# Performance work log

Hardware: AMD Instinct MI355X
Metric: run time of the kernel (lower is better)

Reference implementation:

```python
import functools
import jax, jax.numpy as jnp
import numpy as np

CUTOFF = 5.0
BOX = 80.0
N_POINTS = 8192
MAX_NEIGHBOURS = 32
MASK_VALUE = -1


def setup_inputs() -> dict:
    key = jax.random.key(0)
    positions = jax.random.uniform(key, (N_POINTS, 3), dtype=jnp.float32) * BOX
    return {"positions": positions, "max_neighbours": MAX_NEIGHBOURS}


def reference(positions, max_neighbours):
    # OpenBoundary.get_neighbours (include_self=False, cutoff=CUTOFF)
    n = positions.shape[0]
    # pairwise squared distances: vmap(neighbours_mask_direct) == full broadcast
    diff = positions[:, None, :] - positions[None, :, :]        # [N, N, 3]
    r2 = jnp.sum(diff * diff, axis=-1)                          # [N, N]
    neigh_mask = r2 <= CUTOFF * CUTOFF
    neigh_mask = neigh_mask & ~jnp.eye(n, dtype=bool)           # drop self
    # per-row compaction of hit indices into fixed-size buffer
    get_nb = functools.partial(jnp.argwhere, size=max_neighbours, fill_value=MASK_VALUE)
    to_idx = jax.vmap(get_nb)(neigh_mask)[..., 0]               # [N, max_neighbours]
    cell_indices = jnp.zeros((*to_idx.shape, 3), dtype=jnp.int32)
    actual_max_neighbours = jnp.max(neigh_mask.sum(axis=1))
    return to_idx, cell_indices, actual_max_neighbours
```

## Files before the change

### kernel.cpp

```cpp
#include <hip/hip_runtime.h>


constexpr int   N     = 8192;
constexpr int   MAXNB = 32;
constexpr float CUT2  = 25.0f;
constexpr int   C     = 15;
constexpr int   NCP   = 4096;
constexpr float INVW  = 0.1875f;
constexpr int   QBLOCKS = N / 4;

__device__ __forceinline__ int cell_coord(float v) {
    int c = (int)(v * INVW);
    return c > C - 1 ? C - 1 : c;
}

__global__ __launch_bounds__(1024) void build_kernel(const float* __restrict__ pos,
                                                     int* __restrict__ start_g,
                                                     float4* __restrict__ sorted) {
    __shared__ int cnt[NCP];
    __shared__ int ws[1024];
    const int t = threadIdx.x;

    #pragma unroll
    for (int k = t; k < NCP; k += 1024) cnt[k] = 0;
    __syncthreads();

    int cid[8], rnk[8];
    #pragma unroll
    for (int q = 0; q < 8; ++q) {
        const int i = q * 1024 + t;
        const int cx = cell_coord(pos[3 * i + 0]);
        const int cy = cell_coord(pos[3 * i + 1]);
        const int cz = cell_coord(pos[3 * i + 2]);
        cid[q] = (cz * C + cy) * C + cx;
        rnk[q] = atomicAdd(&cnt[cid[q]], 1);
    }
    __syncthreads();

    int c[4], pre[4], s = 0;
    #pragma unroll
    for (int k = 0; k < 4; ++k) { c[k] = cnt[4 * t + k]; pre[k] = s; s += c[k]; }
    ws[t] = s;
    __syncthreads();
    for (int off = 1; off < 1024; off <<= 1) {
        const int v = (t >= off) ? ws[t - off] : 0;
        __syncthreads();
        ws[t] += v;
        __syncthreads();
    }
    const int excl = ws[t] - s;
    #pragma unroll
    for (int k = 0; k < 4; ++k) {
        cnt[4 * t + k]     = excl + pre[k];
        start_g[4 * t + k] = excl + pre[k];
    }
    if (t == 0) start_g[NCP] = N;
    __syncthreads();

    #pragma unroll
    for (int q = 0; q < 8; ++q) {
        const int i = q * 1024 + t;
        const int p = cnt[cid[q]] + rnk[q];
        sorted[p] = make_float4(pos[3 * i + 0], pos[3 * i + 1], pos[3 * i + 2],
                                __int_as_float(i));
    }
}

__global__ __launch_bounds__(256) void query_kernel(const float* __restrict__ pos,
                                                    const float4* __restrict__ sorted,
                                                    const int* __restrict__ start_g,
                                                    int* __restrict__ out_idx,
                                                    int* __restrict__ blockmax) {
    __shared__ int hitbuf[4][64];
    __shared__ int wmax[4];
    const int lane = threadIdx.x & 63;
    const int wave = threadIdx.x >> 6;
    const int p    = blockIdx.x * 4 + wave;

    const float x = pos[3 * p + 0];
    const float y = pos[3 * p + 1];
    const float z = pos[3 * p + 2];
    const int cx = cell_coord(x), cy = cell_coord(y), cz = cell_coord(z);
    const int xa = cx > 0 ? cx - 1 : 0;
    const int xb = cx < C - 1 ? cx + 1 : C - 1;

    int count = 0;
    #pragma unroll
    for (int s = 0; s < 9; ++s) {
        const int zz = cz + s / 3 - 1;
        const int yy = cy + s % 3 - 1;
        if (zz < 0 || zz >= C || yy < 0 || yy >= C) continue;
        const int rowb = (zz * C + yy) * C;
        const int b = start_g[rowb + xa];
        const int e = start_g[rowb + xb + 1];
        for (int k = b; k < e; k += 64) {
            const int idx = k + lane;
            const float4 o = sorted[idx < N ? idx : N - 1];
            const float dx = __fsub_rn(x, o.x);
            const float dy = __fsub_rn(y, o.y);
            const float dz = __fsub_rn(z, o.z);
            const float r2 = __fadd_rn(__fadd_rn(__fmul_rn(dx, dx), __fmul_rn(dy, dy)),
                                       __fmul_rn(dz, dz));
            const int j = __float_as_int(o.w);
            const bool hit = (idx < e) && (r2 <= CUT2) && (j != p);
            const unsigned long long m = __ballot(hit);
            if (hit) {
                const int pre = __builtin_amdgcn_mbcnt_hi(
                    (unsigned int)(m >> 32),
                    __builtin_amdgcn_mbcnt_lo((unsigned int)m, 0u));
                const int slot = count + pre;
                if (slot < 64) hitbuf[wave][slot] = j;
            }
            count += __popcll(m);
        }
    }

    const int mcount = count < 64 ? count : 64;
    int v = (lane < mcount) ? hitbuf[wave][lane] : 0x7fffffff;
    #pragma unroll
    for (int k = 2; k <= 64; k <<= 1) {
        #pragma unroll
        for (int jj = k >> 1; jj >= 1; jj >>= 1) {
            const int pv = __shfl_xor(v, jj);
            const bool keepmin = ((lane & jj) == 0) == ((lane & k) == 0);
            v = keepmin ? min(v, pv) : max(v, pv);
        }
    }
    if (lane < MAXNB) out_idx[p * MAXNB + lane] = (lane < count) ? v : -1;

    if (lane == 0) wmax[wave] = count;
    __syncthreads();
    if (threadIdx.x == 0)
        blockmax[blockIdx.x] = max(max(wmax[0], wmax[1]), max(wmax[2], wmax[3]));
}

__global__ __launch_bounds__(256) void finalize_kernel(int4* __restrict__ cell4,
                                                       const int* __restrict__ blockmax,
                                                       int* __restrict__ out_max) {
    __shared__ int wm[4];
    const int idx = blockIdx.x * 256 + threadIdx.x;
    cell4[idx] = make_int4(0, 0, 0, 0);
    if (blockIdx.x == 0) {
        int mx = 0;
        for (int k = threadIdx.x; k < QBLOCKS; k += 256) mx = max(mx, blockmax[k]);
        #pragma unroll
        for (int off = 32; off > 0; off >>= 1) mx = max(mx, __shfl_down(mx, off));
        if ((threadIdx.x & 63) == 0) wm[threadIdx.x >> 6] = mx;
        __syncthreads();
        if (threadIdx.x == 0)
            *out_max = max(max(wm[0], wm[1]), max(wm[2], wm[3]));
    }
}

extern "C" void kernel_launch(void* const* d_in, const int* in_sizes, int n_in,
                              void* d_out, int out_size, void* d_ws, size_t ws_size,
                              hipStream_t stream) {
    const float* pos = (const float*)d_in[0];
    int* out = (int*)d_out;

    int* out_idx = out;
    int* base    = out + N * MAXNB;
    int* out_max = out + N * MAXNB * 4;

    int*    start_g = base;
    float4* sorted  = (float4*)(base + 8192);
    int*    blockmax = (int*)d_ws;

    build_kernel   <<<1, 1024, 0, stream>>>(pos, start_g, sorted);
    query_kernel   <<<QBLOCKS, 256, 0, stream>>>(pos, sorted, start_g, out_idx, blockmax);
    finalize_kernel<<<N * MAXNB * 3 / 4 / 256, 256, 0, stream>>>((int4*)base, blockmax, out_max);
}
```

Before: 78.83 us.

## Replace sorted cell list with fixed-capacity cell bins and drop finalize kernel

The build kernel no longer does a block-wide prefix scan to sort points by cell. Each point now goes into a fixed 16-slot bin per cell, and per-cell counts are written to workspace. The query kernel reads a clamped 4x3x3 cell window with one 64-lane load per row instead of variable-length loops. The cell_indices zeroing and the global max are folded into the query kernel, the max via atomicMax, which removes the third launch. The risks are that points beyond 16 per cell are silently dropped and that out_max is never zeroed before the atomicMax.

```diff
diff --git a/kernel.cpp b/kernel.cpp
--- a/kernel.cpp
+++ b/kernel.cpp
@@ -5,9 +5,10 @@
 constexpr int   MAXNB = 32;
 constexpr float CUT2  = 25.0f;
 constexpr int   C     = 15;
-constexpr int   NCP   = 4096;
+constexpr int   NC    = C * C * C;
 constexpr float INVW  = 0.1875f;
-constexpr int   QBLOCKS = N / 4;
+constexpr int   CAPC  = 16;
+constexpr int   QB    = N / 4;
 
 __device__ __forceinline__ int cell_coord(float v) {
     int c = (int)(v * INVW);
@@ -15,62 +16,40 @@
 }
 
 __global__ __launch_bounds__(1024) void build_kernel(const float* __restrict__ pos,
-                                                     int* __restrict__ start_g,
-                                                     float4* __restrict__ sorted) {
-    __shared__ int cnt[NCP];
-    __shared__ int ws[1024];
+                                                     int* __restrict__ cnt_g,
+                                                     float4* __restrict__ cells) {
+    __shared__ int cnt[NC];
     const int t = threadIdx.x;
-
-    #pragma unroll
-    for (int k = t; k < NCP; k += 1024) cnt[k] = 0;
+    for (int k = t; k < NC; k += 1024) cnt[k] = 0;
     __syncthreads();
 
+    float x[8], y[8], z[8];
     int cid[8], rnk[8];
     #pragma unroll
     for (int q = 0; q < 8; ++q) {
         const int i = q * 1024 + t;
-        const int cx = cell_coord(pos[3 * i + 0]);
-        const int cy = cell_coord(pos[3 * i + 1]);
-        const int cz = cell_coord(pos[3 * i + 2]);
-        cid[q] = (cz * C + cy) * C + cx;
+        x[q] = pos[3 * i + 0];
+        y[q] = pos[3 * i + 1];
+        z[q] = pos[3 * i + 2];
+        cid[q] = (cell_coord(z[q]) * C + cell_coord(y[q])) * C + cell_coord(x[q]);
         rnk[q] = atomicAdd(&cnt[cid[q]], 1);
     }
     __syncthreads();
 
-    int c[4], pre[4], s = 0;
-    #pragma unroll
-    for (int k = 0; k < 4; ++k) { c[k] = cnt[4 * t + k]; pre[k] = s; s += c[k]; }
-    ws[t] = s;
-    __syncthreads();
-    for (int off = 1; off < 1024; off <<= 1) {
-        const int v = (t >= off) ? ws[t - off] : 0;
-        __syncthreads();
-        ws[t] += v;
-        __syncthreads();
-    }
-    const int excl = ws[t] - s;
-    #pragma unroll
-    for (int k = 0; k < 4; ++k) {
-        cnt[4 * t + k]     = excl + pre[k];
-        start_g[4 * t + k] = excl + pre[k];
-    }
-    if (t == 0) start_g[NCP] = N;
-    __syncthreads();
-
+    for (int k = t; k < NC; k += 1024) cnt_g[k] = cnt[k];
     #pragma unroll
     for (int q = 0; q < 8; ++q) {
-        const int i = q * 1024 + t;
-        const int p = cnt[cid[q]] + rnk[q];
-        sorted[p] = make_float4(pos[3 * i + 0], pos[3 * i + 1], pos[3 * i + 2],
-                                __int_as_float(i));
+        if (rnk[q] < CAPC)
+            cells[cid[q] * CAPC + rnk[q]] =
+                make_float4(x[q], y[q], z[q], __int_as_float(q * 1024 + t));
     }
 }
 
 __global__ __launch_bounds__(256) void query_kernel(const float* __restrict__ pos,
-                                                    const float4* __restrict__ sorted,
-                                                    const int* __restrict__ start_g,
-                                                    int* __restrict__ out_idx,
-                                                    int* __restrict__ blockmax) {
+                                                    const float4* __restrict__ cells,
+                                                    const int* __restrict__ cnt_g,
+                                                    int* __restrict__ out,
+                                                    int* __restrict__ out_max) {
     __shared__ int hitbuf[4][64];
     __shared__ int wmax[4];
     const int lane = threadIdx.x & 63;
@@ -81,38 +60,38 @@
     const float y = pos[3 * p + 1];
     const float z = pos[3 * p + 2];
     const int cx = cell_coord(x), cy = cell_coord(y), cz = cell_coord(z);
-    const int xa = cx > 0 ? cx - 1 : 0;
-    const int xb = cx < C - 1 ? cx + 1 : C - 1;
+    int xa = cx - 1; xa = xa < 0 ? 0 : (xa > C - 4 ? C - 4 : xa);
+    int ya = cy - 1; ya = ya < 0 ? 0 : (ya > C - 3 ? C - 3 : ya);
+    int za = cz - 1; za = za < 0 ? 0 : (za > C - 3 ? C - 3 : za);
+
+    const int lc = lane >> 4;
+    const int ls = lane & 15;
 
     int count = 0;
     #pragma unroll
     for (int s = 0; s < 9; ++s) {
-        const int zz = cz + s / 3 - 1;
-        const int yy = cy + s % 3 - 1;
-        if (zz < 0 || zz >= C || yy < 0 || yy >= C) continue;
-        const int rowb = (zz * C + yy) * C;
-        const int b = start_g[rowb + xa];
-        const int e = start_g[rowb + xb + 1];
-        for (int k = b; k < e; k += 64) {
-            const int idx = k + lane;
-            const float4 o = sorted[idx < N ? idx : N - 1];
-            const float dx = __fsub_rn(x, o.x);
-            const float dy = __fsub_rn(y, o.y);
-            const float dz = __fsub_rn(z, o.z);
-            const float r2 = __fadd_rn(__fadd_rn(__fmul_rn(dx, dx), __fmul_rn(dy, dy)),
-                                       __fmul_rn(dz, dz));
-            const int j = __float_as_int(o.w);
-            const bool hit = (idx < e) && (r2 <= CUT2) && (j != p);
-            const unsigned long long m = __ballot(hit);
-            if (hit) {
-                const int pre = __builtin_amdgcn_mbcnt_hi(
-                    (unsigned int)(m >> 32),
-                    __builtin_amdgcn_mbcnt_lo((unsigned int)m, 0u));
-                const int slot = count + pre;
-                if (slot < 64) hitbuf[wave][slot] = j;
-            }
-            count += __popcll(m);
+        const int zz = za + s / 3;
+        const int yy = ya + s % 3;
+        const int cidb = (zz * C + yy) * C + xa;
+        const int cid  = cidb + lc;
+        const float4 o = cells[cidb * CAPC + lane];
+        const int   cc = cnt_g[cid];
+        const float dx = __fsub_rn(x, o.x);
+        const float dy = __fsub_rn(y, o.y);
+        const float dz = __fsub_rn(z, o.z);
+        const float r2 = __fadd_rn(__fadd_rn(__fmul_rn(dx, dx), __fmul_rn(dy, dy)),
+                                   __fmul_rn(dz, dz));
+        const int j = __float_as_int(o.w);
+        const bool hit = (ls < cc) && (r2 <= CUT2) && (j != p);
+        const unsigned long long m = __ballot(hit);
+        if (hit) {
+            const int pre = __builtin_amdgcn_mbcnt_hi(
+                (unsigned int)(m >> 32),
+                __builtin_amdgcn_mbcnt_lo((unsigned int)m, 0u));
+            const int slot = count + pre;
+            if (slot < 64) hitbuf[wave][slot] = j;
         }
+        count += __popcll(m);
     }
 
     const int mcount = count < 64 ? count : 64;
@@ -126,30 +105,15 @@
             v = keepmin ? min(v, pv) : max(v, pv);
         }
     }
-    if (lane < MAXNB) out_idx[p * MAXNB + lane] = (lane < count) ? v : -1;
+    if (lane < MAXNB) out[p * MAXNB + lane] = (lane < count) ? v : -1;
+
+    int4* c4 = (int4*)(out + N * MAXNB) + blockIdx.x * 96;
+    if (threadIdx.x < 96) c4[threadIdx.x] = make_int4(0, 0, 0, 0);
 
     if (lane == 0) wmax[wave] = count;
     __syncthreads();
     if (threadIdx.x == 0)
-        blockmax[blockIdx.x] = max(max(wmax[0], wmax[1]), max(wmax[2], wmax[3]));
-}
-
-__global__ __launch_bounds__(256) void finalize_kernel(int4* __restrict__ cell4,
-                                                       const int* __restrict__ blockmax,
-                                                       int* __restrict__ out_max) {
-    __shared__ int wm[4];
-    const int idx = blockIdx.x * 256 + threadIdx.x;
-    cell4[idx] = make_int4(0, 0, 0, 0);
-    if (blockIdx.x == 0) {
-        int mx = 0;
-        for (int k = threadIdx.x; k < QBLOCKS; k += 256) mx = max(mx, blockmax[k]);
-        #pragma unroll
-        for (int off = 32; off > 0; off >>= 1) mx = max(mx, __shfl_down(mx, off));
-        if ((threadIdx.x & 63) == 0) wm[threadIdx.x >> 6] = mx;
-        __syncthreads();
-        if (threadIdx.x == 0)
-            *out_max = max(max(wm[0], wm[1]), max(wm[2], wm[3]));
-    }
+        atomicMax(out_max, max(max(wmax[0], wmax[1]), max(wmax[2], wmax[3])));
 }
 
 extern "C" void kernel_launch(void* const* d_in, const int* in_sizes, int n_in,
@@ -157,16 +121,11 @@
                               hipStream_t stream) {
     const float* pos = (const float*)d_in[0];
     int* out = (int*)d_out;
-
-    int* out_idx = out;
-    int* base    = out + N * MAXNB;
     int* out_max = out + N * MAXNB * 4;
 
-    int*    start_g = base;
-    float4* sorted  = (float4*)(base + 8192);
-    int*    blockmax = (int*)d_ws;
+    int*    cnt_g = (int*)d_ws;
+    float4* cells = (float4*)((char*)d_ws + 16384);
 
-    build_kernel   <<<1, 1024, 0, stream>>>(pos, start_g, sorted);
-    query_kernel   <<<QBLOCKS, 256, 0, stream>>>(pos, sorted, start_g, out_idx, blockmax);
-    finalize_kernel<<<N * MAXNB * 3 / 4 / 256, 256, 0, stream>>>((int4*)base, blockmax, out_max);
+    build_kernel<<<1, 1024, 0, stream>>>(pos, cnt_g, cells);
+    query_kernel<<<QB, 256, 0, stream>>>(pos, cells, cnt_g, out, out_max);
 }
```

Result: slower. 93.12 us (+18.1%).

## Flatten 9 cell-row ranges into one contiguous lane-packed loop

Applied to the files above, without the earlier changes.

The query kernel now precomputes the begin offsets and prefix sums of all nine 3-cell row ranges and loops over their concatenated length in 64-lane chunks. Each lane maps its flat index back to a sorted position with a select chain. This packs partial chunks from different rows together, cutting wasted lanes and loop iterations. The window is also clamped to the grid interior, so edge particles scan a full 3x3x3 block that includes some extra cells. The query index is made wave-uniform with readfirstlane. The cost is nine extra compare/selects per lane per iteration.

```diff
diff --git a/kernel.cpp b/kernel.cpp
--- a/kernel.cpp
+++ b/kernel.cpp
@@ -75,44 +75,52 @@
     __shared__ int wmax[4];
     const int lane = threadIdx.x & 63;
     const int wave = threadIdx.x >> 6;
-    const int p    = blockIdx.x * 4 + wave;
+    const int p = __builtin_amdgcn_readfirstlane((int)blockIdx.x * 4 + wave);
 
     const float x = pos[3 * p + 0];
     const float y = pos[3 * p + 1];
     const float z = pos[3 * p + 2];
     const int cx = cell_coord(x), cy = cell_coord(y), cz = cell_coord(z);
-    const int xa = cx > 0 ? cx - 1 : 0;
-    const int xb = cx < C - 1 ? cx + 1 : C - 1;
+    int xa = cx - 1; xa = xa < 0 ? 0 : (xa > C - 3 ? C - 3 : xa);
+    int ya = cy - 1; ya = ya < 0 ? 0 : (ya > C - 3 ? C - 3 : ya);
+    int za = cz - 1; za = za < 0 ? 0 : (za > C - 3 ? C - 3 : za);
+
+    int bb[9], pre[10];
+    pre[0] = 0;
+    #pragma unroll
+    for (int s = 0; s < 9; ++s) {
+        const int rowb = ((za + s / 3) * C + (ya + s % 3)) * C + xa;
+        bb[s] = start_g[rowb];
+        pre[s + 1] = pre[s] + (start_g[rowb + 3] - bb[s]);
+    }
+    const int total = pre[9];
 
     int count = 0;
-    #pragma unroll
-    for (int s = 0; s < 9; ++s) {
-        const int zz = cz + s / 3 - 1;
-        const int yy = cy + s % 3 - 1;
-        if (zz < 0 || zz >= C || yy < 0 || yy >= C) continue;
-        const int rowb = (zz * C + yy) * C;
-        const int b = start_g[rowb + xa];
-        const int e = start_g[rowb + xb + 1];
-        for (int k = b; k < e; k += 64) {
-            const int idx = k + lane;
-            const float4 o = sorted[idx < N ? idx : N - 1];
-            const float dx = __fsub_rn(x, o.x);
-            const float dy = __fsub_rn(y, o.y);
-            const float dz = __fsub_rn(z, o.z);
-            const float r2 = __fadd_rn(__fadd_rn(__fmul_rn(dx, dx), __fmul_rn(dy, dy)),
-                                       __fmul_rn(dz, dz));
-            const int j = __float_as_int(o.w);
-            const bool hit = (idx < e) && (r2 <= CUT2) && (j != p);
-            const unsigned long long m = __ballot(hit);
-            if (hit) {
-                const int pre = __builtin_amdgcn_mbcnt_hi(
-                    (unsigned int)(m >> 32),
-                    __builtin_amdgcn_mbcnt_lo((unsigned int)m, 0u));
-                const int slot = count + pre;
-                if (slot < 64) hitbuf[wave][slot] = j;
-            }
-            count += __popcll(m);
+    for (int base = 0; base < total; base += 64) {
+        const int l = base + lane;
+        int idx = 0;
+        #pragma unroll
+        for (int s = 0; s < 9; ++s) {
+            const bool in_s = (l >= pre[s]) && (l < pre[s + 1]);
+            idx = in_s ? (bb[s] + (l - pre[s])) : idx;
         }
+        const float4 o = sorted[idx];
+        const float dx = __fsub_rn(x, o.x);
+        const float dy = __fsub_rn(y, o.y);
+        const float dz = __fsub_rn(z, o.z);
+        const float r2 = __fadd_rn(__fadd_rn(__fmul_rn(dx, dx), __fmul_rn(dy, dy)),
+                                   __fmul_rn(dz, dz));
+        const int j = __float_as_int(o.w);
+        const bool hit = (l < total) && (r2 <= CUT2) && (j != p);
+        const unsigned long long m = __ballot(hit);
+        if (hit) {
+            const int pr = __builtin_amdgcn_mbcnt_hi(
+                (unsigned int)(m >> 32),
+                __builtin_amdgcn_mbcnt_lo((unsigned int)m, 0u));
+            const int slot = count + pr;
+            if (slot < 64) hitbuf[wave][slot] = j;
+        }
+        count += __popcll(m);
     }
 
     const int mcount = count < 64 ? count : 64;
@@ -162,8 +170,8 @@
     int* base    = out + N * MAXNB;
     int* out_max = out + N * MAXNB * 4;
 
-    int*    start_g = base;
-    float4* sorted  = (float4*)(base + 8192);
+    int*    start_g  = base;
+    float4* sorted   = (float4*)(base + 8192);
     int*    blockmax = (int*)d_ws;
 
     build_kernel   <<<1, 1024, 0, stream>>>(pos, start_g, sorted);
```

After: 77.11 us. 1.02x faster.
